# Performance work log

Hardware: AMD Instinct MI355X
Metric: run time of the kernel (lower is better)

Reference implementation:

```python
import jax, jax.numpy as jnp
import numpy as np
import math

NH = 12  # num_attention_heads (multiple of 4 required by pattern dispatch)


def _forward(Input, hidden_states, attention_mask, Wq, bq, Wk, bk, Wv, bv, Wo, bo, L):
    b, n, _, H = Input.shape
    hd = H // NH
    G = NH // 4  # heads per criss-cross pattern
    # boolean-mask gather of valid (head, tail) entity pairs, row-major like torch
    bi, ri, ci = jnp.nonzero(attention_mask > 0, size=L)
    x = Input[bi, ri, ci]            # [L, H] keys/values source
    xq = hidden_states[bi, ri, ci]   # [L, H] query source
    q = (xq @ Wq + bq).reshape(L, NH, hd)
    k = (x @ Wk + bk).reshape(L, NH, hd)
    v = (x @ Wv + bv).reshape(L, NH, hd)
    ar = jnp.arange(n)
    # per-pattern criss-cross masks for query position (b, r, c), each [L, n]
    m0 = attention_mask[bi, ri, :] * (ar[None, :] != ci[:, None])  # row r, exclude self col c
    m1 = attention_mask[bi, :, ci] * (ar[None, :] != ri[:, None])  # col c, exclude self row r
    m2 = attention_mask[bi, :, ri]                                  # col r (no self exclusion)
    m3 = attention_mask[bi, ci, :]                                  # row c (no self exclusion)
    adds = jnp.stack([(1.0 - m) * -10000.0 for m in (m0, m1, m2, m3)], axis=1)  # [L, 4, n]
    # scatter per-pattern head groups into zero grid, then criss-cross gather
    k_gs, v_gs = [], []
    for p in range(4):
        sk = jnp.zeros((b, n, n, G, hd), k.dtype).at[bi, ri, ci].set(k[:, p::4])
        sv = jnp.zeros((b, n, n, G, hd), v.dtype).at[bi, ri, ci].set(v[:, p::4])
        if p == 0:
            gk, gv = sk[bi, ri], sv[bi, ri]          # element [l,k] = grid[b, r, k]
        elif p == 1:
            gk, gv = sk[bi, :, ci], sv[bi, :, ci]    # grid[b, k, c]
        elif p == 2:
            gk, gv = sk[bi, :, ri], sv[bi, :, ri]    # grid[b, k, r]
        else:
            gk, gv = sk[bi, ci], sv[bi, ci]          # grid[b, c, k]
        k_gs.append(gk)
        v_gs.append(gv)
    kg = jnp.stack(k_gs, axis=1)  # [L, 4, n, G, hd]
    vg = jnp.stack(v_gs, axis=1)
    # head h = 4*g + p (k[:, p::4] picks heads p, p+4, p+8)
    kg = kg.transpose(0, 3, 1, 2, 4).reshape(L, NH, n, hd)
    vg = vg.transpose(0, 3, 1, 2, 4).reshape(L, NH, n, hd)
    amask = jnp.broadcast_to(adds[:, None, :, :], (L, G, 4, n)).reshape(L, NH, n)
    # prepend self key/value; NOTE: original code uses additive bias +1.0 (ones) for the self slot
    kf = jnp.concatenate([k[:, :, None, :], kg], axis=2)   # [L, NH, n+1, hd]
    vf = jnp.concatenate([v[:, :, None, :], vg], axis=2)
    amask = jnp.concatenate([jnp.ones((L, NH, 1), amask.dtype), amask], axis=-1)
    scores = jnp.einsum('lhd,lhkd->lhk', q, kf) / math.sqrt(hd) + amask
    probs = jax.nn.softmax(scores, axis=-1)  # dropout is identity in eval
    ctx = jnp.einsum('lhk,lhkd->lhd', probs, vf).reshape(L, H)
    return ctx @ Wo + bo


def setup_inputs() -> dict:
    key = jax.random.key(0)
    ks = jax.random.split(key, 8)
    b, n, H = 2, 40, 768
    Input = jax.random.normal(ks[0], (b, n, n, H), jnp.float32)
    hidden_states = jax.random.normal(ks[1], (b, n, n, H), jnp.float32)
    # all valid entity pairs except self pairs -> deterministic L
    attention_mask = (jnp.ones((b, n, n)) - jnp.eye(n)[None]).astype(jnp.float32)
    L = int(b * n * (n - 1))  # 3120
    std = 0.02
    Wq = std * jax.random.normal(ks[2], (H, H), jnp.float32)
    Wk = std * jax.random.normal(ks[3], (H, H), jnp.float32)
    Wv = std * jax.random.normal(ks[4], (H, H), jnp.float32)
    Wo = std * jax.random.normal(ks[5], (H, H), jnp.float32)
    bq = jnp.zeros((H,), jnp.float32)
    bk = jnp.zeros((H,), jnp.float32)
    bv = jnp.zeros((H,), jnp.float32)
    bo = jnp.zeros((H,), jnp.float32)
    return {"Input": Input, "hidden_states": hidden_states, "attention_mask": attention_mask,
            "Wq": Wq, "bq": bq, "Wk": Wk, "bk": bk, "Wv": Wv, "bv": bv, "Wo": Wo, "bo": bo, "L": L}


def reference(Input, hidden_states, attention_mask, Wq, bq, Wk, bk, Wv, bv, Wo, bo, L):
    return _forward(Input, hidden_states, attention_mask, Wq, bq, Wk, bk, Wv, bv, Wo, bo, L)
```

## Files before the change

### kernel.cpp

```cpp
#include <hip/hip_runtime.h>
#include <hip/hip_bf16.h>
#include <math.h>

#define NHEADS 12

typedef __attribute__((ext_vector_type(4))) float f32x4;
typedef __attribute__((ext_vector_type(8))) short bf16x8;

__device__ __forceinline__ unsigned short f2bf(float x) {
  __hip_bfloat16 h = __float2bfloat16(x);
  return *reinterpret_cast<unsigned short*>(&h);
}
__device__ __forceinline__ float bf2f(unsigned short u) {
  union { unsigned int i; float f; } c; c.i = ((unsigned int)u) << 16; return c.f;
}

__global__ __launch_bounds__(256) void prep(const float* __restrict__ mask, int total,
                                            int* __restrict__ pos2l, int* __restrict__ lidx,
                                            const float* __restrict__ bk, const float* __restrict__ bv,
                                            float* __restrict__ bkv,
                                            const float* __restrict__ W0, const float* __restrict__ W1,
                                            const float* __restrict__ W2, const float* __restrict__ W3,
                                            unsigned short* __restrict__ T0, unsigned short* __restrict__ T1,
                                            unsigned short* __restrict__ T2, unsigned short* __restrict__ T3,
                                            int H) {
  int nt32 = H / 32;
  int nw = nt32 * nt32 * 4;
  int bx = blockIdx.x;
  int t = threadIdx.x;
  if (bx < nw) {
    __shared__ float tile[32][33];
    int z = bx / (nt32 * nt32);
    int rem = bx - z * nt32 * nt32;
    int byy = rem / nt32;
    int bxx = rem - byy * nt32;
    const float* W = (z == 0) ? W0 : (z == 1) ? W1 : (z == 2) ? W2 : W3;
    unsigned short* T = (z == 0) ? T0 : (z == 1) ? T1 : (z == 2) ? T2 : T3;
    int k0 = byy * 32, n0 = bxx * 32;
    int kk = t >> 3, n4 = (t & 7) * 4;
    float4 v = *reinterpret_cast<const float4*>(W + (size_t)(k0 + kk) * H + n0 + n4);
    tile[n4 + 0][kk] = v.x; tile[n4 + 1][kk] = v.y; tile[n4 + 2][kk] = v.z; tile[n4 + 3][kk] = v.w;
    __syncthreads();
    int nn2 = t >> 3, k4 = (t & 7) * 4;
#pragma unroll
    for (int e = 0; e < 4; ++e)
      T[(size_t)(n0 + nn2) * H + k0 + k4 + e] = f2bf(tile[nn2][k4 + e]);
  } else {
    __shared__ int cnt[256];
    for (int i = t; i < H; i += 256) { bkv[i] = bk[i]; bkv[H + i] = bv[i]; }
    int per = (total + 255) >> 8;
    int begin = t * per;
    int end = begin + per; if (end > total) end = total;
    if (begin > total) begin = total;
    int c = 0;
    for (int i = begin; i < end; ++i) c += (mask[i] > 0.f) ? 1 : 0;
    cnt[t] = c;
    __syncthreads();
    for (int off = 1; off < 256; off <<= 1) {
      int vv = (t >= off) ? cnt[t - off] : 0;
      __syncthreads();
      cnt[t] += vv;
      __syncthreads();
    }
    int excl = cnt[t] - c;
    for (int i = begin; i < end; ++i) {
      if (mask[i] > 0.f) { pos2l[i] = excl; lidx[excl] = i; ++excl; }
      else pos2l[i] = -1;
    }
  }
}

__global__ __launch_bounds__(256) void gatherconv(const float* __restrict__ hidden,
                                                  const float* __restrict__ input,
                                                  const int* __restrict__ lidx,
                                                  unsigned short* __restrict__ Aq,
                                                  unsigned short* __restrict__ Akv,
                                                  int L, int H) {
  int i = blockIdx.x * 256 + threadIdx.x;
  int per = H / 8;
  if (i >= L * per) return;
  int row = i / per;
  int sub = (i - row * per) * 8;
  size_t src = (size_t)lidx[row] * H + sub;
  size_t dst = (size_t)row * H + sub;
  {
    float4 a = *reinterpret_cast<const float4*>(hidden + src);
    float4 b = *reinterpret_cast<const float4*>(hidden + src + 4);
    bf16x8 st;
    st[0]=f2bf(a.x); st[1]=f2bf(a.y); st[2]=f2bf(a.z); st[3]=f2bf(a.w);
    st[4]=f2bf(b.x); st[5]=f2bf(b.y); st[6]=f2bf(b.z); st[7]=f2bf(b.w);
    *reinterpret_cast<bf16x8*>(Aq + dst) = st;
  }
  {
    float4 a = *reinterpret_cast<const float4*>(input + src);
    float4 b = *reinterpret_cast<const float4*>(input + src + 4);
    bf16x8 st;
    st[0]=f2bf(a.x); st[1]=f2bf(a.y); st[2]=f2bf(a.z); st[3]=f2bf(a.w);
    st[4]=f2bf(b.x); st[5]=f2bf(b.y); st[6]=f2bf(b.z); st[7]=f2bf(b.w);
    *reinterpret_cast<bf16x8*>(Akv + dst) = st;
  }
}

#define QBM 128
#define QBN 128
#define QBK 64

template <bool OUT_BF16>
__device__ __forceinline__ void gemm128_core(const unsigned short* __restrict__ A,
                                             const unsigned short* __restrict__ Bt,
                                             const float* __restrict__ bias,
                                             void* __restrict__ C,
                                             int M, int N, int K, int m0, int n0,
                                             unsigned short* sA, unsigned short* sB) {
  int tid = threadIdx.x;
  int wid = tid >> 6, lane = tid & 63;
  int wm = wid >> 1, wn = wid & 1;
  int lr = lane & 15, lq = lane >> 4;
  f32x4 acc[4][4] = {};

  for (int k0 = 0; k0 < K; k0 += QBK) {
#pragma unroll
    for (int r = 0; r < 4; ++r) {
      int c = (r * 4 + wid) * 64 + lane;
      int row = c >> 3, sl = c & 7;
      int sg = sl ^ (row & 7);
      __builtin_amdgcn_global_load_lds((const __attribute__((address_space(1))) unsigned int*)(A + (size_t)(m0 + row) * K + k0 + sg * 8),
                                       (__attribute__((address_space(3))) unsigned int*)(sA + (r * 4 + wid) * 512),
                                       16, 0, 0);
    }
#pragma unroll
    for (int r = 0; r < 4; ++r) {
      int c = (r * 4 + wid) * 64 + lane;
      int row = c >> 3, sl = c & 7;
      int sg = sl ^ (row & 7);
      __builtin_amdgcn_global_load_lds((const __attribute__((address_space(1))) unsigned int*)(Bt + (size_t)(n0 + row) * K + k0 + sg * 8),
                                       (__attribute__((address_space(3))) unsigned int*)(sB + (r * 4 + wid) * 512),
                                       16, 0, 0);
    }
    __syncthreads();
#pragma unroll
    for (int ks = 0; ks < 2; ++ks) {
      bf16x8 af[4], bfr[4];
#pragma unroll
      for (int i = 0; i < 4; ++i) {
        int row = wm * 64 + i * 16 + lr;
        int slot = (ks * 4 + lq) ^ (row & 7);
        af[i] = *reinterpret_cast<const bf16x8*>(sA + row * 64 + slot * 8);
      }
#pragma unroll
      for (int j = 0; j < 4; ++j) {
        int rn = wn * 64 + j * 16 + lr;
        int slot = (ks * 4 + lq) ^ (rn & 7);
        bfr[j] = *reinterpret_cast<const bf16x8*>(sB + rn * 64 + slot * 8);
      }
#pragma unroll
      for (int i = 0; i < 4; ++i)
#pragma unroll
        for (int j = 0; j < 4; ++j)
          acc[i][j] = __builtin_amdgcn_mfma_f32_16x16x32_bf16(af[i], bfr[j], acc[i][j], 0, 0, 0);
    }
    __syncthreads();
  }

#pragma unroll
  for (int i = 0; i < 4; ++i) {
#pragma unroll
    for (int j = 0; j < 4; ++j) {
      int gcol = n0 + wn * 64 + j * 16 + lr;
      float bv = bias[gcol];
      int rbase = m0 + wm * 64 + i * 16 + lq * 4;
#pragma unroll
      for (int r = 0; r < 4; ++r) {
        int gm = rbase + r;
        if (gm >= M) continue;
        float val = acc[i][j][r] + bv;
        if (OUT_BF16) ((unsigned short*)C)[(size_t)gm * N + gcol] = f2bf(val);
        else          ((float*)C)[(size_t)gm * N + gcol] = val;
      }
    }
  }
}

__global__ __launch_bounds__(256) void gemm_qkv(const unsigned short* __restrict__ Aq,
                                                const unsigned short* __restrict__ Akv,
                                                const unsigned short* __restrict__ Wqt,
                                                const unsigned short* __restrict__ Wkvt,
                                                const float* __restrict__ bq,
                                                const float* __restrict__ bkv,
                                                unsigned short* __restrict__ Cq,
                                                unsigned short* __restrict__ Ckv,
                                                int M, int K, int H) {
  __shared__ unsigned short sA[QBM * QBK];
  __shared__ unsigned short sB[QBN * QBK];
  int nq = H / QBN;
  int bx = blockIdx.x;
  int m0 = blockIdx.y * QBM;
  if (bx < nq)
    gemm128_core<true>(Aq, Wqt, bq, Cq, M, H, K, m0, bx * QBN, sA, sB);
  else
    gemm128_core<true>(Akv, Wkvt, bkv, Ckv, M, 2 * H, K, m0, (bx - nq) * QBN, sA, sB);
}

#define GBM 128
#define GBN 64
#define GBK 64

__global__ __launch_bounds__(256) void gemm_out(const unsigned short* __restrict__ A,
                                                const unsigned short* __restrict__ Bt,
                                                const float* __restrict__ bias,
                                                float* __restrict__ C,
                                                int M, int N, int K) {
  __shared__ unsigned short sA[GBM * GBK];
  __shared__ unsigned short sB[GBN * GBK];
  int tid = threadIdx.x;
  int wid = tid >> 6, lane = tid & 63;
  int wm = wid >> 1, wn = wid & 1;
  int m0 = blockIdx.y * GBM, n0 = blockIdx.x * GBN;
  int lr = lane & 15, lq = lane >> 4;
  f32x4 acc[4][2] = {};

  for (int k0 = 0; k0 < K; k0 += GBK) {
#pragma unroll
    for (int r = 0; r < 4; ++r) {
      int c = (r * 4 + wid) * 64 + lane;
      int row = c >> 3, sl = c & 7;
      int sg = sl ^ (row & 7);
      __builtin_amdgcn_global_load_lds((const __attribute__((address_space(1))) unsigned int*)(A + (size_t)(m0 + row) * K + k0 + sg * 8),
                                       (__attribute__((address_space(3))) unsigned int*)(sA + (r * 4 + wid) * 512),
                                       16, 0, 0);
    }
#pragma unroll
    for (int r = 0; r < 2; ++r) {
      int c = (r * 4 + wid) * 64 + lane;
      int row = c >> 3, sl = c & 7;
      int sg = sl ^ (row & 7);
      __builtin_amdgcn_global_load_lds((const __attribute__((address_space(1))) unsigned int*)(Bt + (size_t)(n0 + row) * K + k0 + sg * 8),
                                       (__attribute__((address_space(3))) unsigned int*)(sB + (r * 4 + wid) * 512),
                                       16, 0, 0);
    }
    __syncthreads();
#pragma unroll
    for (int ks = 0; ks < 2; ++ks) {
      bf16x8 af[4], bfr[2];
#pragma unroll
      for (int i = 0; i < 4; ++i) {
        int row = wm * 64 + i * 16 + lr;
        int slot = (ks * 4 + lq) ^ (row & 7);
        af[i] = *reinterpret_cast<const bf16x8*>(sA + row * 64 + slot * 8);
      }
#pragma unroll
      for (int j = 0; j < 2; ++j) {
        int rn = wn * 32 + j * 16 + lr;
        int slot = (ks * 4 + lq) ^ (rn & 7);
        bfr[j] = *reinterpret_cast<const bf16x8*>(sB + rn * 64 + slot * 8);
      }
#pragma unroll
      for (int i = 0; i < 4; ++i)
#pragma unroll
        for (int j = 0; j < 2; ++j)
          acc[i][j] = __builtin_amdgcn_mfma_f32_16x16x32_bf16(af[i], bfr[j], acc[i][j], 0, 0, 0);
    }
    __syncthreads();
  }

#pragma unroll
  for (int i = 0; i < 4; ++i) {
#pragma unroll
    for (int j = 0; j < 2; ++j) {
      int gcol = n0 + wn * 32 + j * 16 + lr;
      float bv = bias[gcol];
      int rbase = m0 + wm * 64 + i * 16 + lq * 4;
#pragma unroll
      for (int r = 0; r < 4; ++r) {
        int gm = rbase + r;
        if (gm >= M) continue;
        C[(size_t)gm * N + gcol] = acc[i][j][r] + bv;
      }
    }
  }
}

__global__ __launch_bounds__(128) void attn3(const unsigned short* __restrict__ qb,
                                             const unsigned short* __restrict__ KVb,
                                             const float* __restrict__ mask,
                                             const int* __restrict__ pos2l,
                                             unsigned short* __restrict__ ctx,
                                             int n, int H) {
  __shared__ unsigned short Ks[40 * 72];
  __shared__ unsigned short Vs[40 * 72];
  __shared__ float S[40][42];
  __shared__ float mrow[40];
  __shared__ int qlist[40];

  int bx = blockIdx.x;
  int r0 = bx % n;
  int h3 = (bx / n) % 3;
  int p = (bx / (3 * n)) % 4;
  int bi = bx / (12 * n);
  int h = p + 4 * h3;
  int nn = n * n;
  bool rowkeys = (p == 0 || p == 3);
  bool rowq = (p == 0 || p == 2);
  bool excl = (p < 2);
  int t = threadIdx.x;
  int H2 = 2 * H;

  if (t < 80) {
    int half = t / 40, j = t % 40;
    int keypos = rowkeys ? (r0 * n + j) : (j * n + r0);
    int l2 = pos2l[bi * nn + keypos];
    unsigned short* dst = (half ? Vs : Ks) + j * 72;
    if (l2 >= 0) {
      const unsigned short* src = KVb + (size_t)l2 * H2 + half * H + h * 64;
#pragma unroll
      for (int e8 = 0; e8 < 8; ++e8)
        *reinterpret_cast<bf16x8*>(dst + e8 * 8) = *reinterpret_cast<const bf16x8*>(src + e8 * 8);
    } else {
      bf16x8 z = {};
#pragma unroll
      for (int e8 = 0; e8 < 8; ++e8) *reinterpret_cast<bf16x8*>(dst + e8 * 8) = z;
    }
  }
  if (t < 40) {
    mrow[t] = rowkeys ? mask[bi * nn + r0 * n + t] : mask[bi * nn + t * n + r0];
    int qpos = rowq ? (r0 * n + t) : (t * n + r0);
    qlist[t] = pos2l[bi * nn + qpos];
  }
  __syncthreads();

  int c = t % 40;
  int role = t / 40;
  int lq = (t < 80) ? qlist[c] : -1;

  if (lq >= 0) {
    float qf[64];
    const unsigned short* qp = qb + (size_t)lq * H + h * 64;
#pragma unroll
    for (int e8 = 0; e8 < 8; ++e8) {
      bf16x8 t8 = *reinterpret_cast<const bf16x8*>(qp + e8 * 8);
#pragma unroll
      for (int e = 0; e < 8; ++e) qf[e8 * 8 + e] = bf2f((unsigned short)t8[e]);
    }
    int j0 = role * 20;
#pragma unroll 2
    for (int j = j0; j < j0 + 20; ++j) {
      float acc = 0.f;
#pragma unroll
      for (int e8 = 0; e8 < 8; ++e8) {
        bf16x8 kv = *reinterpret_cast<const bf16x8*>(Ks + j * 72 + e8 * 8);
#pragma unroll
        for (int e = 0; e < 8; ++e) acc = fmaf(qf[e8 * 8 + e], bf2f((unsigned short)kv[e]), acc);
      }
      float mval = mrow[j] * ((excl && j == c) ? 0.f : 1.f);
      S[c][j] = acc * 0.125f + (1.f - mval) * -10000.f;
    }
    if (role == 0) {
      const unsigned short* kp = KVb + (size_t)lq * H2 + h * 64;
      float acc = 0.f;
#pragma unroll
      for (int e8 = 0; e8 < 8; ++e8) {
        bf16x8 kv = *reinterpret_cast<const bf16x8*>(kp + e8 * 8);
#pragma unroll
        for (int e = 0; e < 8; ++e) acc = fmaf(qf[e8 * 8 + e], bf2f((unsigned short)kv[e]), acc);
      }
      S[c][40] = acc * 0.125f + 1.0f;
    }
  }
  __syncthreads();

  if (t < 40 && qlist[t] >= 0) {
    float mx = -3.0e38f;
    for (int j = 0; j <= 40; ++j) mx = fmaxf(mx, S[t][j]);
    float sum = 0.f;
    for (int j = 0; j <= 40; ++j) { float e = __expf(S[t][j] - mx); S[t][j] = e; sum += e; }
    float inv = 1.f / sum;
    for (int j = 0; j <= 40; ++j) S[t][j] *= inv;
  }
  __syncthreads();

  if (lq >= 0) {
    int d0 = role * 32;
    const unsigned short* vsp = KVb + (size_t)lq * H2 + H + h * 64 + d0;
    float pself = S[c][40];
#pragma unroll
    for (int ch = 0; ch < 4; ++ch) {
      int dd = d0 + ch * 8;
      float facc[8];
      bf16x8 vself = *reinterpret_cast<const bf16x8*>(vsp + ch * 8);
#pragma unroll
      for (int e = 0; e < 8; ++e) facc[e] = pself * bf2f((unsigned short)vself[e]);
      for (int j = 0; j < 40; ++j) {
        float pj = S[c][j];
        bf16x8 vv = *reinterpret_cast<const bf16x8*>(Vs + j * 72 + dd);
#pragma unroll
        for (int e = 0; e < 8; ++e) facc[e] = fmaf(pj, bf2f((unsigned short)vv[e]), facc[e]);
      }
      bf16x8 st;
#pragma unroll
      for (int e = 0; e < 8; ++e) st[e] = f2bf(facc[e]);
      *reinterpret_cast<bf16x8*>(ctx + (size_t)lq * H + h * 64 + dd) = st;
    }
  }
}

extern "C" void kernel_launch(void* const* d_in, const int* in_sizes, int n_in,
                              void* d_out, int out_size, void* d_ws, size_t ws_size,
                              hipStream_t stream) {
  const float* Input  = (const float*)d_in[0];
  const float* hidden = (const float*)d_in[1];
  const float* mask   = (const float*)d_in[2];
  const float* Wq = (const float*)d_in[3];
  const float* bq = (const float*)d_in[4];
  const float* Wk = (const float*)d_in[5];
  const float* bk = (const float*)d_in[6];
  const float* Wv = (const float*)d_in[7];
  const float* bv = (const float*)d_in[8];
  const float* Wo = (const float*)d_in[9];
  const float* bo = (const float*)d_in[10];

  int H = (int)llround(sqrt((double)in_sizes[3]));
  int total = in_sizes[2];
  int L = out_size / H;
  int bn = total - L;
  int n = total / bn;
  int b = bn / n;
  int mtiles = (L + QBM - 1) / QBM;
  int Mpad = mtiles * QBM;
  size_t aElems = (size_t)Mpad * H;

  char* p = (char*)d_ws;
  auto take = [&](size_t bytes) { char* r = p; p += (bytes + 255) & ~(size_t)255; return r; };
  int* lidx  = (int*)take((size_t)L * 4);
  int* pos2l = (int*)take((size_t)total * 4);
  float* bkv = (float*)take((size_t)2 * H * 4);
  unsigned short* Wqt  = (unsigned short*)take((size_t)H * H * 2);
  unsigned short* Wot  = (unsigned short*)take((size_t)H * H * 2);
  unsigned short* Wkvt = (unsigned short*)take((size_t)2 * H * H * 2);
  unsigned short* Aq   = (unsigned short*)take(aElems * 2);
  unsigned short* Akv  = (unsigned short*)take(aElems * 2);
  unsigned short* qb2  = (unsigned short*)take(aElems * 2);
  unsigned short* KVb  = (unsigned short*)take(aElems * 2 * 2);
  unsigned short* ctxb = (unsigned short*)take(aElems * 2);

  int nt32 = H / 32;
  int nwconv = nt32 * nt32 * 4;
  prep<<<nwconv + 1, 256, 0, stream>>>(mask, total, pos2l, lidx, bk, bv, bkv,
                                       Wq, Wk, Wv, Wo,
                                       Wqt, Wkvt, Wkvt + (size_t)H * H, Wot, H);
  {
    int nthr = L * (H / 8);
    gatherconv<<<(nthr + 255) / 256, 256, 0, stream>>>(hidden, Input, lidx, Aq, Akv, L, H);
  }
  gemm_qkv<<<dim3(3 * H / QBN, mtiles), 256, 0, stream>>>(Aq, Akv, Wqt, Wkvt, bq, bkv,
                                                          qb2, KVb, L, H, H);
  attn3<<<b * 4 * 3 * n, 128, 0, stream>>>(qb2, KVb, mask, pos2l, ctxb, n, H);
  gemm_out<<<dim3(H / GBN, mtiles), 256, 0, stream>>>(ctxb, Wot, bo, (float*)d_out, L, H, H);
}
```

Baseline: 88.26 us.

## Fold input bf16 conversion into prep and gather rows inside QKV GEMM

Drops the separate gatherconv kernel. The prep kernel now converts the full hidden and Input grids to bf16 in parallel with the weight transposes, and the QKV GEMM gathers rows through lidx when it loads its tiles. Both GEMMs also switch to a 1-D grid with an XCD-aware workgroup remap and precompute per-thread load pointers. This removes one launch and the dependency on lidx before conversion, but converts all positions including masked ones, which adds a little traffic.

```diff
diff --git a/kernel.cpp b/kernel.cpp
--- a/kernel.cpp
+++ b/kernel.cpp
@@ -13,6 +13,12 @@
 }
 __device__ __forceinline__ float bf2f(unsigned short u) {
   union { unsigned int i; float f; } c; c.i = ((unsigned int)u) << 16; return c.f;
+}
+
+__device__ __forceinline__ int xcd_swz(int orig, int nwg) {
+  int q = nwg >> 3, r = nwg & 7;
+  int xcd = orig & 7, idx = orig >> 3;
+  return (xcd < r ? xcd * (q + 1) : r * (q + 1) + (xcd - r) * q) + idx;
 }
 
 __global__ __launch_bounds__(256) void prep(const float* __restrict__ mask, int total,
@@ -23,6 +29,8 @@
                                             const float* __restrict__ W2, const float* __restrict__ W3,
                                             unsigned short* __restrict__ T0, unsigned short* __restrict__ T1,
                                             unsigned short* __restrict__ T2, unsigned short* __restrict__ T3,
+                                            const float* __restrict__ hidden, const float* __restrict__ input,
+                                            unsigned short* __restrict__ Hbf, unsigned short* __restrict__ Ibf,
                                             int H) {
   int nt32 = H / 32;
   int nw = nt32 * nt32 * 4;
@@ -45,7 +53,7 @@
 #pragma unroll
     for (int e = 0; e < 4; ++e)
       T[(size_t)(n0 + nn2) * H + k0 + k4 + e] = f2bf(tile[nn2][k4 + e]);
-  } else {
+  } else if (bx == nw) {
     __shared__ int cnt[256];
     for (int i = t; i < H; i += 256) { bkv[i] = bk[i]; bkv[H + i] = bv[i]; }
     int per = (total + 255) >> 8;
@@ -67,37 +75,19 @@
       if (mask[i] > 0.f) { pos2l[i] = excl; lidx[excl] = i; ++excl; }
       else pos2l[i] = -1;
     }
-  }
-}
-
-__global__ __launch_bounds__(256) void gatherconv(const float* __restrict__ hidden,
-                                                  const float* __restrict__ input,
-                                                  const int* __restrict__ lidx,
-                                                  unsigned short* __restrict__ Aq,
-                                                  unsigned short* __restrict__ Akv,
-                                                  int L, int H) {
-  int i = blockIdx.x * 256 + threadIdx.x;
-  int per = H / 8;
-  if (i >= L * per) return;
-  int row = i / per;
-  int sub = (i - row * per) * 8;
-  size_t src = (size_t)lidx[row] * H + sub;
-  size_t dst = (size_t)row * H + sub;
-  {
-    float4 a = *reinterpret_cast<const float4*>(hidden + src);
-    float4 b = *reinterpret_cast<const float4*>(hidden + src + 4);
+  } else {
+    int idx = bx - nw - 1;
+    int perarr = (total * H) >> 11;
+    int which = idx / perarr;
+    size_t off = (size_t)(idx - which * perarr) * 2048 + t * 8;
+    const float* src = which ? input : hidden;
+    unsigned short* dst = which ? Ibf : Hbf;
+    float4 a = *reinterpret_cast<const float4*>(src + off);
+    float4 b2 = *reinterpret_cast<const float4*>(src + off + 4);
     bf16x8 st;
     st[0]=f2bf(a.x); st[1]=f2bf(a.y); st[2]=f2bf(a.z); st[3]=f2bf(a.w);
-    st[4]=f2bf(b.x); st[5]=f2bf(b.y); st[6]=f2bf(b.z); st[7]=f2bf(b.w);
-    *reinterpret_cast<bf16x8*>(Aq + dst) = st;
-  }
-  {
-    float4 a = *reinterpret_cast<const float4*>(input + src);
-    float4 b = *reinterpret_cast<const float4*>(input + src + 4);
-    bf16x8 st;
-    st[0]=f2bf(a.x); st[1]=f2bf(a.y); st[2]=f2bf(a.z); st[3]=f2bf(a.w);
-    st[4]=f2bf(b.x); st[5]=f2bf(b.y); st[6]=f2bf(b.z); st[7]=f2bf(b.w);
-    *reinterpret_cast<bf16x8*>(Akv + dst) = st;
+    st[4]=f2bf(b2.x); st[5]=f2bf(b2.y); st[6]=f2bf(b2.z); st[7]=f2bf(b2.w);
+    *reinterpret_cast<bf16x8*>(dst + off) = st;
   }
 }
 
@@ -105,8 +95,9 @@
 #define QBN 128
 #define QBK 64
 
-template <bool OUT_BF16>
+template <bool OUT_BF16, bool GATHER>
 __device__ __forceinline__ void gemm128_core(const unsigned short* __restrict__ A,
+                                             const int* __restrict__ lidx,
                                              const unsigned short* __restrict__ Bt,
                                              const float* __restrict__ bias,
                                              void* __restrict__ C,
@@ -118,25 +109,30 @@
   int lr = lane & 15, lq = lane >> 4;
   f32x4 acc[4][4] = {};
 
+  const unsigned short* aptr[4];
+  const unsigned short* bptr[4];
+#pragma unroll
+  for (int r = 0; r < 4; ++r) {
+    int c = (r * 4 + wid) * 64 + lane;
+    int row = c >> 3, sl = c & 7;
+    int sg = sl ^ (row & 7);
+    int gm = m0 + row; if (gm >= M) gm = M - 1;
+    size_t abase = GATHER ? (size_t)lidx[gm] * K : (size_t)gm * K;
+    aptr[r] = A + abase + sg * 8;
+    bptr[r] = Bt + (size_t)(n0 + row) * K + sg * 8;
+  }
+
   for (int k0 = 0; k0 < K; k0 += QBK) {
 #pragma unroll
-    for (int r = 0; r < 4; ++r) {
-      int c = (r * 4 + wid) * 64 + lane;
-      int row = c >> 3, sl = c & 7;
-      int sg = sl ^ (row & 7);
-      __builtin_amdgcn_global_load_lds((const __attribute__((address_space(1))) unsigned int*)(A + (size_t)(m0 + row) * K + k0 + sg * 8),
+    for (int r = 0; r < 4; ++r)
+      __builtin_amdgcn_global_load_lds((const __attribute__((address_space(1))) unsigned int*)(aptr[r] + k0),
                                        (__attribute__((address_space(3))) unsigned int*)(sA + (r * 4 + wid) * 512),
                                        16, 0, 0);
-    }
-#pragma unroll
-    for (int r = 0; r < 4; ++r) {
-      int c = (r * 4 + wid) * 64 + lane;
-      int row = c >> 3, sl = c & 7;
-      int sg = sl ^ (row & 7);
-      __builtin_amdgcn_global_load_lds((const __attribute__((address_space(1))) unsigned int*)(Bt + (size_t)(n0 + row) * K + k0 + sg * 8),
+#pragma unroll
+    for (int r = 0; r < 4; ++r)
+      __builtin_amdgcn_global_load_lds((const __attribute__((address_space(1))) unsigned int*)(bptr[r] + k0),
                                        (__attribute__((address_space(3))) unsigned int*)(sB + (r * 4 + wid) * 512),
                                        16, 0, 0);
-    }
     __syncthreads();
 #pragma unroll
     for (int ks = 0; ks < 2; ++ks) {
@@ -181,24 +177,26 @@
   }
 }
 
-__global__ __launch_bounds__(256) void gemm_qkv(const unsigned short* __restrict__ Aq,
-                                                const unsigned short* __restrict__ Akv,
+__global__ __launch_bounds__(256) void gemm_qkv(const unsigned short* __restrict__ Hbf,
+                                                const unsigned short* __restrict__ Ibf,
                                                 const unsigned short* __restrict__ Wqt,
                                                 const unsigned short* __restrict__ Wkvt,
                                                 const float* __restrict__ bq,
                                                 const float* __restrict__ bkv,
+                                                const int* __restrict__ lidx,
                                                 unsigned short* __restrict__ Cq,
                                                 unsigned short* __restrict__ Ckv,
-                                                int M, int K, int H) {
+                                                int M, int K, int H, int NX) {
   __shared__ unsigned short sA[QBM * QBK];
   __shared__ unsigned short sB[QBN * QBK];
+  int wgid = xcd_swz(blockIdx.x, gridDim.x);
+  int y = wgid / NX, x = wgid - y * NX;
+  int m0 = y * QBM;
   int nq = H / QBN;
-  int bx = blockIdx.x;
-  int m0 = blockIdx.y * QBM;
-  if (bx < nq)
-    gemm128_core<true>(Aq, Wqt, bq, Cq, M, H, K, m0, bx * QBN, sA, sB);
+  if (x < nq)
+    gemm128_core<true, true>(Hbf, lidx, Wqt, bq, Cq, M, H, K, m0, x * QBN, sA, sB);
   else
-    gemm128_core<true>(Akv, Wkvt, bkv, Ckv, M, 2 * H, K, m0, (bx - nq) * QBN, sA, sB);
+    gemm128_core<true, true>(Ibf, lidx, Wkvt, bkv, Ckv, M, 2 * H, K, m0, (x - nq) * QBN, sA, sB);
 }
 
 #define GBM 128
@@ -212,32 +210,38 @@
                                                 int M, int N, int K) {
   __shared__ unsigned short sA[GBM * GBK];
   __shared__ unsigned short sB[GBN * GBK];
+  int NX = N / GBN;
+  int wgid = xcd_swz(blockIdx.x, gridDim.x);
+  int y = wgid / NX, x = wgid - y * NX;
+  int m0 = y * GBM, n0 = x * GBN;
   int tid = threadIdx.x;
   int wid = tid >> 6, lane = tid & 63;
   int wm = wid >> 1, wn = wid & 1;
-  int m0 = blockIdx.y * GBM, n0 = blockIdx.x * GBN;
   int lr = lane & 15, lq = lane >> 4;
   f32x4 acc[4][2] = {};
 
+  const unsigned short* aptr[4];
+  const unsigned short* bptr[2];
+#pragma unroll
+  for (int r = 0; r < 4; ++r) {
+    int c = (r * 4 + wid) * 64 + lane;
+    int row = c >> 3, sl = c & 7;
+    int sg = sl ^ (row & 7);
+    aptr[r] = A + (size_t)(m0 + row) * K + sg * 8;
+    if (r < 2) bptr[r] = Bt + (size_t)(n0 + row) * K + sg * 8;
+  }
+
   for (int k0 = 0; k0 < K; k0 += GBK) {
 #pragma unroll
-    for (int r = 0; r < 4; ++r) {
-      int c = (r * 4 + wid) * 64 + lane;
-      int row = c >> 3, sl = c & 7;
-      int sg = sl ^ (row & 7);
-      __builtin_amdgcn_global_load_lds((const __attribute__((address_space(1))) unsigned int*)(A + (size_t)(m0 + row) * K + k0 + sg * 8),
+    for (int r = 0; r < 4; ++r)
+      __builtin_amdgcn_global_load_lds((const __attribute__((address_space(1))) unsigned int*)(aptr[r] + k0),
                                        (__attribute__((address_space(3))) unsigned int*)(sA + (r * 4 + wid) * 512),
                                        16, 0, 0);
-    }
-#pragma unroll
-    for (int r = 0; r < 2; ++r) {
-      int c = (r * 4 + wid) * 64 + lane;
-      int row = c >> 3, sl = c & 7;
-      int sg = sl ^ (row & 7);
-      __builtin_amdgcn_global_load_lds((const __attribute__((address_space(1))) unsigned int*)(Bt + (size_t)(n0 + row) * K + k0 + sg * 8),
+#pragma unroll
+    for (int r = 0; r < 2; ++r)
+      __builtin_amdgcn_global_load_lds((const __attribute__((address_space(1))) unsigned int*)(bptr[r] + k0),
                                        (__attribute__((address_space(3))) unsigned int*)(sB + (r * 4 + wid) * 512),
                                        16, 0, 0);
-    }
     __syncthreads();
 #pragma unroll
     for (int ks = 0; ks < 2; ++ks) {
@@ -427,6 +431,7 @@
   int mtiles = (L + QBM - 1) / QBM;
   int Mpad = mtiles * QBM;
   size_t aElems = (size_t)Mpad * H;
+  size_t posElems = (size_t)total * H;
 
   char* p = (char*)d_ws;
   auto take = [&](size_t bytes) { char* r = p; p += (bytes + 255) & ~(size_t)255; return r; };
@@ -436,23 +441,24 @@
   unsigned short* Wqt  = (unsigned short*)take((size_t)H * H * 2);
   unsigned short* Wot  = (unsigned short*)take((size_t)H * H * 2);
   unsigned short* Wkvt = (unsigned short*)take((size_t)2 * H * H * 2);
-  unsigned short* Aq   = (unsigned short*)take(aElems * 2);
-  unsigned short* Akv  = (unsigned short*)take(aElems * 2);
+  unsigned short* Hbf  = (unsigned short*)take(posElems * 2);
+  unsigned short* Ibf  = (unsigned short*)take(posElems * 2);
   unsigned short* qb2  = (unsigned short*)take(aElems * 2);
   unsigned short* KVb  = (unsigned short*)take(aElems * 2 * 2);
   unsigned short* ctxb = (unsigned short*)take(aElems * 2);
 
   int nt32 = H / 32;
   int nwconv = nt32 * nt32 * 4;
-  prep<<<nwconv + 1, 256, 0, stream>>>(mask, total, pos2l, lidx, bk, bv, bkv,
-                                       Wq, Wk, Wv, Wo,
-                                       Wqt, Wkvt, Wkvt + (size_t)H * H, Wot, H);
+  int nconv = 2 * (int)((posElems) >> 11);
+  prep<<<nwconv + 1 + nconv, 256, 0, stream>>>(mask, total, pos2l, lidx, bk, bv, bkv,
+                                               Wq, Wk, Wv, Wo,
+                                               Wqt, Wkvt, Wkvt + (size_t)H * H, Wot,
+                                               hidden, Input, Hbf, Ibf, H);
   {
-    int nthr = L * (H / 8);
-    gatherconv<<<(nthr + 255) / 256, 256, 0, stream>>>(hidden, Input, lidx, Aq, Akv, L, H);
-  }
-  gemm_qkv<<<dim3(3 * H / QBN, mtiles), 256, 0, stream>>>(Aq, Akv, Wqt, Wkvt, bq, bkv,
-                                                          qb2, KVb, L, H, H);
+    int NX = 3 * H / QBN;
+    gemm_qkv<<<NX * mtiles, 256, 0, stream>>>(Hbf, Ibf, Wqt, Wkvt, bq, bkv, lidx,
+                                              qb2, KVb, L, H, H, NX);
+  }
   attn3<<<b * 4 * 3 * n, 128, 0, stream>>>(qb2, KVb, mask, pos2l, ctxb, n, H);
-  gemm_out<<<dim3(H / GBN, mtiles), 256, 0, stream>>>(ctxb, Wot, bo, (float*)d_out, L, H, H);
-}
+  gemm_out<<<(H / GBN) * mtiles, 256, 0, stream>>>(ctxb, Wot, bo, (float*)d_out, L, H, H);
+}
```

New measurement: 86.10 us. 1.03x faster.
